# Kernel optimization log

Hardware: AMD Instinct MI355X
Metric: run time of the kernel (lower is better)

Reference implementation:

```python
import jax, jax.numpy as jnp
import numpy as np

DIM = 1024
HEADS = 16


def setup_inputs() -> dict:
    key = jax.random.key(0)
    ks = jax.random.split(key, 5)
    x = jax.random.normal(ks[0], (2, 2048, DIM), dtype=jnp.float32)
    # nn.Linear init-like scaling
    qkv_w = jax.random.normal(ks[1], (3 * DIM, DIM), dtype=jnp.float32) * (1.0 / np.sqrt(DIM))
    qkv_b = jax.random.normal(ks[2], (3 * DIM,), dtype=jnp.float32) * 0.02
    proj_w = jax.random.normal(ks[3], (DIM, DIM), dtype=jnp.float32) * (1.0 / np.sqrt(DIM))
    proj_b = jax.random.normal(ks[4], (DIM,), dtype=jnp.float32) * 0.02
    return {"x": x, "qkv_w": qkv_w, "qkv_b": qkv_b, "proj_w": proj_w, "proj_b": proj_b}


def reference(x, qkv_w, qkv_b, proj_w, proj_b):
    B, N, C = x.shape
    H = HEADS
    Dh = C // H
    scale = Dh ** -0.5
    # qkv: [B, N, 3C] -> [3, B, H, N, Dh]
    qkv = (x @ qkv_w.T + qkv_b).reshape(B, N, 3, H, Dh).transpose(2, 0, 3, 1, 4)
    q, k, v = qkv[0], qkv[1], qkv[2]
    attn = jnp.einsum('bhnd,bhmd->bhnm', q, k) * scale
    attn = jax.nn.softmax(attn, axis=-1)
    out = jnp.einsum('bhnm,bhmd->bhnd', attn, v)  # [B, H, N, Dh]
    out = out.transpose(0, 2, 1, 3).reshape(B, N, C)
    return out @ proj_w.T + proj_b
```

## Files before the change

### kernel.cpp

```cpp
#include <hip/hip_runtime.h>
#include <stdint.h>

#define DIM    1024
#define NHEADS 16
#define DH     64
#define SEQ    2048
#define BATCH  2
#define BHEADS (BATCH * NHEADS)
#define MROWS  (BATCH * SEQ)
#define SL2E   0.18033688011112042f

typedef __attribute__((ext_vector_type(8))) short bf16x8;
typedef __attribute__((ext_vector_type(4))) float f32x4;
typedef __attribute__((ext_vector_type(16))) float f32x16;
typedef unsigned short ushort_t;

#define GLDS(gp, lp) __builtin_amdgcn_global_load_lds( \
    (__attribute__((address_space(1))) void*)(gp), \
    (__attribute__((address_space(3))) void*)(lp), 16, 0, 0)

__device__ inline ushort_t f2bf(float f) {
    unsigned u = __builtin_bit_cast(unsigned, f);
    u += 0x7FFFu + ((u >> 16) & 1u);
    return (ushort_t)(u >> 16);
}

__global__ __launch_bounds__(256) void cvt_kernel(
    const float* __restrict__ s0, const float* __restrict__ s1, const float* __restrict__ s2,
    ushort_t* __restrict__ d0, ushort_t* __restrict__ d1, ushort_t* __restrict__ d2)
{
    const int N0 = MROWS * DIM;
    const int N1 = 3 * DIM * DIM;
    const int N2 = DIM * DIM;
    int e = (blockIdx.x * 256 + threadIdx.x) << 2;
    const float* src; ushort_t* dst;
    if (e < N0)                { src = s0 + e;             dst = d0 + e; }
    else if (e < N0 + N1)      { src = s1 + (e - N0);      dst = d1 + (e - N0); }
    else if (e < N0 + N1 + N2) { src = s2 + (e - N0 - N1); dst = d2 + (e - N0 - N1); }
    else return;
    float4 f = *(const float4*)src;
    ushort4 o;
    o.x = f2bf(f.x); o.y = f2bf(f.y); o.z = f2bf(f.z); o.w = f2bf(f.w);
    *(ushort4*)dst = o;
}

__global__ __launch_bounds__(256) void qkv_gemm(
    const ushort_t* __restrict__ A, const ushort_t* __restrict__ W,
    const float* __restrict__ bias,
    ushort_t* __restrict__ Qw, ushort_t* __restrict__ Kw, ushort_t* __restrict__ Vt)
{
    __shared__ union {
        ushort_t stage[2][2][128 * 64];
        ushort_t T[128 * 136];
    } sm;

    const int tid  = threadIdx.x;
    const int lane = tid & 63;
    const int wave = tid >> 6;
    const int quad = lane >> 4;
    const int l16  = lane & 15;
    const int wm   = (wave >> 1) * 64;
    const int wn   = (wave & 1) * 64;
    const int bm   = blockIdx.x * 128;
    const int bn   = blockIdx.y * 128;
    const int Rl   = lane >> 3;
    const int pp   = lane & 7;

    f32x4 acc[4][4];
    for (int i = 0; i < 4; i++)
        for (int j = 0; j < 4; j++)
            for (int r = 0; r < 4; r++) acc[i][j][r] = 0.f;

    for (int j = 0; j < 4; j++) {
        int Rb = j * 32 + wave * 8;
        int R  = Rb + Rl;
        int c  = pp ^ (R & 7);
        GLDS(A + (size_t)(bm + R) * DIM + c * 8, sm.stage[0][0] + Rb * 64 + lane * 8);
        GLDS(W + (size_t)(bn + R) * DIM + c * 8, sm.stage[0][1] + Rb * 64 + lane * 8);
    }

    const int NT = DIM / 64;
    for (int t = 0; t < NT; t++) {
        if (t < NT - 1) {
            int kk = (t + 1) * 64;
            ushort_t* As1 = sm.stage[(t + 1) & 1][0];
            ushort_t* Bs1 = sm.stage[(t + 1) & 1][1];
            for (int j = 0; j < 4; j++) {
                int Rb = j * 32 + wave * 8;
                int R  = Rb + Rl;
                int c  = pp ^ (R & 7);
                GLDS(A + (size_t)(bm + R) * DIM + kk + c * 8, As1 + Rb * 64 + lane * 8);
                GLDS(W + (size_t)(bn + R) * DIM + kk + c * 8, Bs1 + Rb * 64 + lane * 8);
            }
            __asm volatile("s_waitcnt vmcnt(8)" ::: "memory");
        } else {
            __asm volatile("s_waitcnt vmcnt(0)" ::: "memory");
        }
        __asm volatile("s_barrier" ::: "memory");

        const ushort_t* Asb = sm.stage[t & 1][0];
        const ushort_t* Bsb = sm.stage[t & 1][1];
        for (int kh = 0; kh < 2; kh++) {
            bf16x8 a[4], b[4];
            for (int mi = 0; mi < 4; mi++) {
                int r = wm + mi * 16 + l16;
                a[mi] = *(const bf16x8*)(Asb + r * 64 + (((kh * 4 + quad) ^ (r & 7)) << 3));
            }
            for (int ni = 0; ni < 4; ni++) {
                int r = wn + ni * 16 + l16;
                b[ni] = *(const bf16x8*)(Bsb + r * 64 + (((kh * 4 + quad) ^ (r & 7)) << 3));
            }
            for (int mi = 0; mi < 4; mi++)
                for (int ni = 0; ni < 4; ni++)
                    acc[mi][ni] = __builtin_amdgcn_mfma_f32_16x16x32_bf16(a[mi], b[ni], acc[mi][ni], 0, 0, 0);
        }
        __asm volatile("s_waitcnt lgkmcnt(0)" ::: "memory");
        __asm volatile("s_barrier" ::: "memory");
    }

    const int three = bn >> 10;
    const float scale = (three == 0) ? SL2E : 1.0f;
    for (int ni = 0; ni < 4; ni++) {
        int cl   = wn + ni * 16 + l16;
        float bv = bias[bn + cl];
        for (int mi = 0; mi < 4; mi++)
            for (int reg = 0; reg < 4; reg++) {
                int r = wm + mi * 16 + quad * 4 + reg;
                sm.T[r * 136 + cl] = f2bf((acc[mi][ni][reg] + bv) * scale);
            }
    }
    __syncthreads();

    const int b = bm >> 11, npos0 = bm & 2047;
    if (three < 2) {
        int r = tid >> 1, hh = tid & 1;
        int hc = (bn + hh * 64) & 1023;
        int h  = hc >> 6;
        ushort_t* dst = (three == 0 ? Qw : Kw) + ((size_t)(b * NHEADS + h) * SEQ + npos0 + r) * DH;
        const ushort_t* srcp = sm.T + r * 136 + hh * 64;
        for (int s = 0; s < 8; s++)
            *(uint4*)(dst + s * 8) = *(const uint4*)(srcp + s * 8);
    } else {
        int c = tid & 127, hh = tid >> 7;
        int hc = (bn + c) & 1023;
        int h  = hc >> 6, d = hc & 63;
        ushort_t* dst = Vt + ((size_t)(b * NHEADS + h) * DH + d) * SEQ + npos0 + hh * 64;
        for (int s = 0; s < 8; s++) {
            union { ushort_t u[8]; uint4 v; } tmp;
            for (int k2 = 0; k2 < 8; k2++) {
                int o  = hh * 64 + s * 8 + k2;
                int po = (o & ~12) | ((o & 4) << 1) | ((o & 8) >> 1);
                tmp.u[k2] = sm.T[po * 136 + c];
            }
            *(uint4*)(dst + s * 8) = tmp.v;
        }
    }
}

struct AttnSmem {
    ushort_t Qs[128 * 64];
    ushort_t Ks[3][2][32 * 64];
    ushort_t Vs[3][64 * 64];
};
union AttnSmemU {
    AttnSmem m;
    float Lb[128][66];
};

__global__ __launch_bounds__(512, 4) void attn_kernel(
    const ushort_t* __restrict__ Qw, const ushort_t* __restrict__ Kw,
    const ushort_t* __restrict__ Vt, ushort_t* __restrict__ Ao)
{
    __shared__ AttnSmemU sh;

    const int tid  = threadIdx.x;
    const int lane = tid & 63;
    const int wave = tid >> 6;
    const int grp  = wave >> 2;
    const int wg   = wave & 3;
    const int hi   = lane >> 5;
    const int l32  = lane & 31;
    const int Rl   = lane >> 3;
    const int pp   = lane & 7;

    const int bid  = blockIdx.x + 16 * blockIdx.y;
    const int bid2 = (bid & 7) * 64 + (bid >> 3);
    const int bh   = bid2 >> 4;
    const int q0   = (bid2 & 15) * 128;

    const ushort_t* Qh = Qw + (size_t)bh * SEQ * DH;
    const ushort_t* Kh = Kw + (size_t)bh * SEQ * DH;
    const ushort_t* Vh = Vt + (size_t)bh * DH * SEQ;

    for (int j = 0; j < 2; j++) {
        int Rb = j * 64 + wave * 8;
        int R  = Rb + Rl;
        int c  = pp ^ (R & 7);
        GLDS(Qh + (size_t)(q0 + R) * DH + c * 8, sh.m.Qs + Rb * 64 + lane * 8);
    }
    {
        int R = wg * 8 + Rl;
        int c = pp ^ (R & 7);
        GLDS(Kh + (size_t)(grp * 32 + R) * DH + c * 8, sh.m.Ks[0][grp] + wg * 512 + lane * 8);
        int Rd = wave * 8 + Rl;
        int cv = pp ^ (Rd & 7);
        GLDS(Vh + (size_t)Rd * SEQ + cv * 8, sh.m.Vs[0] + wave * 512 + lane * 8);
    }

    f32x16 oacc[2], liD, SZERO;
#pragma unroll
    for (int i = 0; i < 16; i++) { oacc[0][i] = 0.f; oacc[1][i] = 0.f; liD[i] = 0.f; SZERO[i] = 0.f; }
    bf16x8 qf[4];
    bf16x8 vones;
#pragma unroll
    for (int i = 0; i < 8; i++) vones[i] = (short)0x3F80;

    const int NIT = 32;
    int cur = 0;
    for (int it = 0; it < NIT; it++) {
        if (it < NIT - 1) {
            int nb = cur + 1; if (nb == 3) nb = 0;
            int kb = (it + 1) * 64;
            int R  = wg * 8 + Rl;
            int c  = pp ^ (R & 7);
            GLDS(Kh + (size_t)(kb + grp * 32 + R) * DH + c * 8, sh.m.Ks[nb][grp] + wg * 512 + lane * 8);
            int Rd = wave * 8 + Rl;
            int cv = pp ^ (Rd & 7);
            GLDS(Vh + (size_t)Rd * SEQ + kb + cv * 8, sh.m.Vs[nb] + wg * 512 + (grp * 2048) + lane * 8);
            __asm volatile("s_waitcnt vmcnt(2)" ::: "memory");
        } else {
            __asm volatile("s_waitcnt vmcnt(0)" ::: "memory");
        }
        __asm volatile("s_barrier" ::: "memory");

        if (it == 0) {
            int qr = wg * 32 + l32;
#pragma unroll
            for (int kt = 0; kt < 4; kt++)
                qf[kt] = *(const bf16x8*)(sh.m.Qs + qr * 64 + (((2 * kt + hi) ^ (qr & 7)) << 3));
        }

        const ushort_t* Ksb = sh.m.Ks[cur][grp];
        const ushort_t* Vsb = sh.m.Vs[cur];

        f32x16 S;
        __builtin_amdgcn_s_setprio(1);
#pragma unroll
        for (int kt = 0; kt < 4; kt++) {
            bf16x8 kf = *(const bf16x8*)(Ksb + l32 * 64 + (((2 * kt + hi) ^ (l32 & 7)) << 3));
            S = __builtin_amdgcn_mfma_f32_32x32x16_bf16(kf, qf[kt], kt == 0 ? SZERO : S, 0, 0, 0);
        }
        __builtin_amdgcn_s_setprio(0);

        unsigned Dw[8];
#pragma unroll
        for (int m = 0; m < 8; m++) {
            float p0 = __builtin_amdgcn_exp2f(S[2 * m]);
            float p1 = __builtin_amdgcn_exp2f(S[2 * m + 1]);
            unsigned d;
            asm("v_cvt_pk_bf16_f32 %0, %1, %2" : "=v"(d) : "v"(p0), "v"(p1));
            Dw[m] = d;
        }
        union { unsigned u[4]; bf16x8 v; } pc0, pc1;
        pc0.u[0] = Dw[0]; pc0.u[1] = Dw[1]; pc0.u[2] = Dw[2]; pc0.u[3] = Dw[3];
        pc1.u[0] = Dw[4]; pc1.u[1] = Dw[5]; pc1.u[2] = Dw[6]; pc1.u[3] = Dw[7];
        bf16x8 pa[2] = { pc0.v, pc1.v };

        __builtin_amdgcn_s_setprio(1);
        liD = __builtin_amdgcn_mfma_f32_32x32x16_bf16(pa[0], vones, liD, 0, 0, 0);
        liD = __builtin_amdgcn_mfma_f32_32x32x16_bf16(pa[1], vones, liD, 0, 0, 0);
#pragma unroll
        for (int kt = 0; kt < 2; kt++)
#pragma unroll
            for (int dh = 0; dh < 2; dh++) {
                int dr = dh * 32 + l32;
                bf16x8 vf = *(const bf16x8*)(Vsb + dr * 64 + (((grp * 4 + 2 * kt + hi) ^ (dr & 7)) << 3));
                oacc[dh] = __builtin_amdgcn_mfma_f32_32x32x16_bf16(pa[kt], vf, oacc[dh], 0, 0, 0);
            }
        __builtin_amdgcn_s_setprio(0);

        cur++; if (cur == 3) cur = 0;
    }

    __syncthreads();

    const int b = bh >> 4, h = bh & 15;
    if (grp == 1) {
#pragma unroll
        for (int dh = 0; dh < 2; dh++)
#pragma unroll
            for (int reg = 0; reg < 16; reg++) {
                int row = wg * 32 + (reg & 3) + 8 * (reg >> 2) + 4 * hi;
                sh.Lb[row][dh * 32 + l32] = oacc[dh][reg];
            }
        if (l32 == 0) {
#pragma unroll
            for (int reg = 0; reg < 16; reg++) {
                int row = wg * 32 + (reg & 3) + 8 * (reg >> 2) + 4 * hi;
                sh.Lb[row][64] = liD[reg];
            }
        }
    }
    __syncthreads();
    if (grp == 0) {
#pragma unroll
        for (int reg = 0; reg < 16; reg++) {
            int row = wg * 32 + (reg & 3) + 8 * (reg >> 2) + 4 * hi;
            float inv = 1.0f / (liD[reg] + sh.Lb[row][64]);
            int grow = q0 + row;
#pragma unroll
            for (int dh = 0; dh < 2; dh++) {
                float o = oacc[dh][reg] + sh.Lb[row][dh * 32 + l32];
                Ao[((size_t)b * SEQ + grow) * DIM + h * 64 + dh * 32 + l32] = f2bf(o * inv);
            }
        }
    }
}

__global__ __launch_bounds__(256, 4) void proj_gemm(
    const ushort_t* __restrict__ A, const ushort_t* __restrict__ W,
    const float* __restrict__ bias, float* __restrict__ Cout)
{
    __shared__ ushort_t Asd[2][128 * 64];
    __shared__ ushort_t Bsd[2][64 * 64];

    const int tid  = threadIdx.x;
    const int lane = tid & 63;
    const int wave = tid >> 6;
    const int quad = lane >> 4;
    const int l16  = lane & 15;
    const int wm   = (wave >> 1) * 64;
    const int wn   = (wave & 1) * 32;
    const int bm   = blockIdx.x * 128;
    const int bn   = blockIdx.y * 64;
    const int Rl   = lane >> 3;
    const int pp   = lane & 7;

    f32x4 acc[4][2];
    for (int i = 0; i < 4; i++)
        for (int j = 0; j < 2; j++)
            for (int r = 0; r < 4; r++) acc[i][j][r] = 0.f;

    for (int j = 0; j < 4; j++) {
        int Rb = j * 32 + wave * 8;
        int R  = Rb + Rl;
        int c  = pp ^ (R & 7);
        GLDS(A + (size_t)(bm + R) * DIM + c * 8, Asd[0] + Rb * 64 + lane * 8);
    }
    for (int j = 0; j < 2; j++) {
        int Rb = j * 32 + wave * 8;
        int R  = Rb + Rl;
        int c  = pp ^ (R & 7);
        GLDS(W + (size_t)(bn + R) * DIM + c * 8, Bsd[0] + Rb * 64 + lane * 8);
    }

    const int NT = DIM / 64;
    for (int t = 0; t < NT; t++) {
        if (t < NT - 1) {
            int kk = (t + 1) * 64;
            ushort_t* As1 = Asd[(t + 1) & 1];
            ushort_t* Bs1 = Bsd[(t + 1) & 1];
            for (int j = 0; j < 4; j++) {
                int Rb = j * 32 + wave * 8;
                int R  = Rb + Rl;
                int c  = pp ^ (R & 7);
                GLDS(A + (size_t)(bm + R) * DIM + kk + c * 8, As1 + Rb * 64 + lane * 8);
            }
            for (int j = 0; j < 2; j++) {
                int Rb = j * 32 + wave * 8;
                int R  = Rb + Rl;
                int c  = pp ^ (R & 7);
                GLDS(W + (size_t)(bn + R) * DIM + kk + c * 8, Bs1 + Rb * 64 + lane * 8);
            }
            __asm volatile("s_waitcnt vmcnt(6)" ::: "memory");
        } else {
            __asm volatile("s_waitcnt vmcnt(0)" ::: "memory");
        }
        __asm volatile("s_barrier" ::: "memory");

        const ushort_t* Asb = Asd[t & 1];
        const ushort_t* Bsb = Bsd[t & 1];
        for (int kh = 0; kh < 2; kh++) {
            bf16x8 a[4], b[2];
            for (int mi = 0; mi < 4; mi++) {
                int r = wm + mi * 16 + l16;
                a[mi] = *(const bf16x8*)(Asb + r * 64 + (((kh * 4 + quad) ^ (r & 7)) << 3));
            }
            for (int ni = 0; ni < 2; ni++) {
                int r = wn + ni * 16 + l16;
                b[ni] = *(const bf16x8*)(Bsb + r * 64 + (((kh * 4 + quad) ^ (r & 7)) << 3));
            }
            for (int mi = 0; mi < 4; mi++)
                for (int ni = 0; ni < 2; ni++)
                    acc[mi][ni] = __builtin_amdgcn_mfma_f32_16x16x32_bf16(a[mi], b[ni], acc[mi][ni], 0, 0, 0);
        }
        __asm volatile("s_waitcnt lgkmcnt(0)" ::: "memory");
        __asm volatile("s_barrier" ::: "memory");
    }

    for (int mi = 0; mi < 4; mi++) {
        for (int ni = 0; ni < 2; ni++) {
            int col  = bn + wn + ni * 16 + l16;
            float bv = bias[col];
            for (int reg = 0; reg < 4; reg++) {
                int row = bm + wm + mi * 16 + quad * 4 + reg;
                Cout[(size_t)row * DIM + col] = acc[mi][ni][reg] + bv;
            }
        }
    }
}

extern "C" void kernel_launch(void* const* d_in, const int* in_sizes, int n_in,
                              void* d_out, int out_size, void* d_ws, size_t ws_size,
                              hipStream_t stream) {
    const float* x      = (const float*)d_in[0];
    const float* qkv_w  = (const float*)d_in[1];
    const float* qkv_b  = (const float*)d_in[2];
    const float* proj_w = (const float*)d_in[3];
    const float* proj_b = (const float*)d_in[4];
    float* out = (float*)d_out;

    ushort_t* xb      = (ushort_t*)d_ws;
    ushort_t* qkv_wb  = xb      + (size_t)MROWS * DIM;
    ushort_t* proj_wb = qkv_wb  + (size_t)3 * DIM * DIM;
    ushort_t* Qw      = proj_wb + (size_t)DIM * DIM;
    ushort_t* Kw      = Qw      + (size_t)BHEADS * SEQ * DH;
    ushort_t* Vt      = Kw      + (size_t)BHEADS * SEQ * DH;
    ushort_t* Ao      = Vt      + (size_t)BHEADS * SEQ * DH;

    const int total_cvt = MROWS * DIM + 3 * DIM * DIM + DIM * DIM;
    cvt_kernel<<<total_cvt / (4 * 256), 256, 0, stream>>>(x, qkv_w, proj_w, xb, qkv_wb, proj_wb);
    qkv_gemm<<<dim3(MROWS / 128, (3 * DIM) / 128), 256, 0, stream>>>(xb, qkv_wb, qkv_b, Qw, Kw, Vt);
    attn_kernel<<<dim3(SEQ / 128, BHEADS), 512, 0, stream>>>(Qw, Kw, Vt, Ao);
    proj_gemm<<<dim3(MROWS / 128, DIM / 64), 256, 0, stream>>>(Ao, proj_wb, proj_b, out);
}
```

Measured before the change: 177.2 us.

## Double-buffer 128-key tiles in attention loop instead of triple-buffered 64-key tiles

The attention kernel's K/V staging moves from a three-stage ring of 64-key tiles to a two-stage double buffer of 128-key tiles. The loop runs 16 iterations instead of 32, each processing two 32-key sub-blocks per wave group. This halves the number of barriers and loop-control overheads. The load for the next tile is now issued after a full vmcnt(0) wait and barrier, which gives less prefetch depth. LDS use grows from about 56KB to 80KB, which may reduce occupancy against the launch bound of 4 blocks.

```diff
diff --git a/kernel.cpp b/kernel.cpp
--- a/kernel.cpp
+++ b/kernel.cpp
@@ -159,8 +159,8 @@
 
 struct AttnSmem {
     ushort_t Qs[128 * 64];
-    ushort_t Ks[3][2][32 * 64];
-    ushort_t Vs[3][64 * 64];
+    ushort_t Ks[2][2][64 * 64];
+    ushort_t Vs[2][64 * 128];
 };
 union AttnSmemU {
     AttnSmem m;
@@ -199,12 +199,18 @@
         GLDS(Qh + (size_t)(q0 + R) * DH + c * 8, sh.m.Qs + Rb * 64 + lane * 8);
     }
     {
-        int R = wg * 8 + Rl;
-        int c = pp ^ (R & 7);
-        GLDS(Kh + (size_t)(grp * 32 + R) * DH + c * 8, sh.m.Ks[0][grp] + wg * 512 + lane * 8);
-        int Rd = wave * 8 + Rl;
-        int cv = pp ^ (Rd & 7);
-        GLDS(Vh + (size_t)Rd * SEQ + cv * 8, sh.m.Vs[0] + wave * 512 + lane * 8);
+        for (int j = 0; j < 2; j++) {
+            int R = wg * 16 + j * 8 + Rl;
+            int c = pp ^ (R & 7);
+            GLDS(Kh + (size_t)(grp * 64 + R) * DH + c * 8,
+                 sh.m.Ks[0][grp] + (wg * 16 + j * 8) * 64 + lane * 8);
+        }
+        for (int j = 0; j < 2; j++) {
+            int Rv = wave * 8 + j * 4 + (lane >> 4);
+            int ck = lane & 15;
+            GLDS(Vh + (size_t)Rv * SEQ + (ck ^ (Rv & 7)) * 8,
+                 sh.m.Vs[0] + (wave * 8 + j * 4) * 128 + lane * 8);
+        }
     }
 
     f32x16 oacc[2], liD, SZERO;
@@ -215,23 +221,27 @@
 #pragma unroll
     for (int i = 0; i < 8; i++) vones[i] = (short)0x3F80;
 
-    const int NIT = 32;
-    int cur = 0;
+    const int NIT = 16;
     for (int it = 0; it < NIT; it++) {
+        __asm volatile("s_waitcnt vmcnt(0)" ::: "memory");
+        __asm volatile("s_barrier" ::: "memory");
+
         if (it < NIT - 1) {
-            int nb = cur + 1; if (nb == 3) nb = 0;
-            int kb = (it + 1) * 64;
-            int R  = wg * 8 + Rl;
-            int c  = pp ^ (R & 7);
-            GLDS(Kh + (size_t)(kb + grp * 32 + R) * DH + c * 8, sh.m.Ks[nb][grp] + wg * 512 + lane * 8);
-            int Rd = wave * 8 + Rl;
-            int cv = pp ^ (Rd & 7);
-            GLDS(Vh + (size_t)Rd * SEQ + kb + cv * 8, sh.m.Vs[nb] + wg * 512 + (grp * 2048) + lane * 8);
-            __asm volatile("s_waitcnt vmcnt(2)" ::: "memory");
-        } else {
-            __asm volatile("s_waitcnt vmcnt(0)" ::: "memory");
-        }
-        __asm volatile("s_barrier" ::: "memory");
+            int nb = (it + 1) & 1;
+            int kb = (it + 1) * 128;
+            for (int j = 0; j < 2; j++) {
+                int R = wg * 16 + j * 8 + Rl;
+                int c = pp ^ (R & 7);
+                GLDS(Kh + (size_t)(kb + grp * 64 + R) * DH + c * 8,
+                     sh.m.Ks[nb][grp] + (wg * 16 + j * 8) * 64 + lane * 8);
+            }
+            for (int j = 0; j < 2; j++) {
+                int Rv = wave * 8 + j * 4 + (lane >> 4);
+                int ck = lane & 15;
+                GLDS(Vh + (size_t)Rv * SEQ + kb + (ck ^ (Rv & 7)) * 8,
+                     sh.m.Vs[nb] + (wave * 8 + j * 4) * 128 + lane * 8);
+            }
+        }
 
         if (it == 0) {
             int qr = wg * 32 + l32;
@@ -240,46 +250,48 @@
                 qf[kt] = *(const bf16x8*)(sh.m.Qs + qr * 64 + (((2 * kt + hi) ^ (qr & 7)) << 3));
         }
 
-        const ushort_t* Ksb = sh.m.Ks[cur][grp];
-        const ushort_t* Vsb = sh.m.Vs[cur];
-
-        f32x16 S;
-        __builtin_amdgcn_s_setprio(1);
-#pragma unroll
-        for (int kt = 0; kt < 4; kt++) {
-            bf16x8 kf = *(const bf16x8*)(Ksb + l32 * 64 + (((2 * kt + hi) ^ (l32 & 7)) << 3));
-            S = __builtin_amdgcn_mfma_f32_32x32x16_bf16(kf, qf[kt], kt == 0 ? SZERO : S, 0, 0, 0);
-        }
-        __builtin_amdgcn_s_setprio(0);
-
-        unsigned Dw[8];
-#pragma unroll
-        for (int m = 0; m < 8; m++) {
-            float p0 = __builtin_amdgcn_exp2f(S[2 * m]);
-            float p1 = __builtin_amdgcn_exp2f(S[2 * m + 1]);
-            unsigned d;
-            asm("v_cvt_pk_bf16_f32 %0, %1, %2" : "=v"(d) : "v"(p0), "v"(p1));
-            Dw[m] = d;
-        }
-        union { unsigned u[4]; bf16x8 v; } pc0, pc1;
-        pc0.u[0] = Dw[0]; pc0.u[1] = Dw[1]; pc0.u[2] = Dw[2]; pc0.u[3] = Dw[3];
-        pc1.u[0] = Dw[4]; pc1.u[1] = Dw[5]; pc1.u[2] = Dw[6]; pc1.u[3] = Dw[7];
-        bf16x8 pa[2] = { pc0.v, pc1.v };
-
-        __builtin_amdgcn_s_setprio(1);
-        liD = __builtin_amdgcn_mfma_f32_32x32x16_bf16(pa[0], vones, liD, 0, 0, 0);
-        liD = __builtin_amdgcn_mfma_f32_32x32x16_bf16(pa[1], vones, liD, 0, 0, 0);
-#pragma unroll
-        for (int kt = 0; kt < 2; kt++)
-#pragma unroll
-            for (int dh = 0; dh < 2; dh++) {
-                int dr = dh * 32 + l32;
-                bf16x8 vf = *(const bf16x8*)(Vsb + dr * 64 + (((grp * 4 + 2 * kt + hi) ^ (dr & 7)) << 3));
-                oacc[dh] = __builtin_amdgcn_mfma_f32_32x32x16_bf16(pa[kt], vf, oacc[dh], 0, 0, 0);
-            }
-        __builtin_amdgcn_s_setprio(0);
-
-        cur++; if (cur == 3) cur = 0;
+        const ushort_t* Ksb = sh.m.Ks[it & 1][grp];
+        const ushort_t* Vsb = sh.m.Vs[it & 1];
+
+#pragma unroll
+        for (int ks = 0; ks < 2; ks++) {
+            f32x16 S;
+            __builtin_amdgcn_s_setprio(1);
+#pragma unroll
+            for (int kt = 0; kt < 4; kt++) {
+                bf16x8 kf = *(const bf16x8*)(Ksb + (ks * 32 + l32) * 64 + (((2 * kt + hi) ^ (l32 & 7)) << 3));
+                S = __builtin_amdgcn_mfma_f32_32x32x16_bf16(kf, qf[kt], kt == 0 ? SZERO : S, 0, 0, 0);
+            }
+            __builtin_amdgcn_s_setprio(0);
+
+            unsigned Dw[8];
+#pragma unroll
+            for (int m = 0; m < 8; m++) {
+                float p0 = __builtin_amdgcn_exp2f(S[2 * m]);
+                float p1 = __builtin_amdgcn_exp2f(S[2 * m + 1]);
+                unsigned d;
+                asm("v_cvt_pk_bf16_f32 %0, %1, %2" : "=v"(d) : "v"(p0), "v"(p1));
+                Dw[m] = d;
+            }
+            union { unsigned u[4]; bf16x8 v; } pc0, pc1;
+            pc0.u[0] = Dw[0]; pc0.u[1] = Dw[1]; pc0.u[2] = Dw[2]; pc0.u[3] = Dw[3];
+            pc1.u[0] = Dw[4]; pc1.u[1] = Dw[5]; pc1.u[2] = Dw[6]; pc1.u[3] = Dw[7];
+            bf16x8 pa[2] = { pc0.v, pc1.v };
+
+            __builtin_amdgcn_s_setprio(1);
+            liD = __builtin_amdgcn_mfma_f32_32x32x16_bf16(pa[0], vones, liD, 0, 0, 0);
+            liD = __builtin_amdgcn_mfma_f32_32x32x16_bf16(pa[1], vones, liD, 0, 0, 0);
+#pragma unroll
+            for (int kt = 0; kt < 2; kt++)
+#pragma unroll
+                for (int dh = 0; dh < 2; dh++) {
+                    int dr = dh * 32 + l32;
+                    int jc = grp * 8 + ks * 4 + 2 * kt + hi;
+                    bf16x8 vf = *(const bf16x8*)(Vsb + dr * 128 + ((jc ^ (l32 & 7)) << 3));
+                    oacc[dh] = __builtin_amdgcn_mfma_f32_32x32x16_bf16(pa[kt], vf, oacc[dh], 0, 0, 0);
+                }
+            __builtin_amdgcn_s_setprio(0);
+        }
     }
 
     __syncthreads();
```

Measured after the change: 178.4 us. Within noise of the previous version (+0.6%).

## Alias Q staging into the third K/V buffer to shrink attention LDS

Applied to the files above, without the earlier changes.

Flattens attention shared memory into one buffer where the Q tile shares space with the third K/V ring slot. Q fragments are loaded into registers before the loop, and tiles 0 and 1 are prefetched up front so slot 2 is free to overwrite. This cuts LDS per block from 64KB to 48KB, and the launch bound is raised to allow higher occupancy. The tighter register budget may cause spills, and with only 512 blocks the extra resident blocks per CU may add little.

```diff
diff --git a/kernel.cpp b/kernel.cpp
--- a/kernel.cpp
+++ b/kernel.cpp
@@ -157,21 +157,14 @@
     }
 }
 
-struct AttnSmem {
-    ushort_t Qs[128 * 64];
-    ushort_t Ks[3][2][32 * 64];
-    ushort_t Vs[3][64 * 64];
-};
-union AttnSmemU {
-    AttnSmem m;
-    float Lb[128][66];
-};
-
-__global__ __launch_bounds__(512, 4) void attn_kernel(
+__global__ __launch_bounds__(512, 6) void attn_kernel(
     const ushort_t* __restrict__ Qw, const ushort_t* __restrict__ Kw,
     const ushort_t* __restrict__ Vt, ushort_t* __restrict__ Ao)
 {
-    __shared__ AttnSmemU sh;
+    __shared__ union {
+        ushort_t u[24576];
+        float Lb[128][66];
+    } sh;
 
     const int tid  = threadIdx.x;
     const int lane = tid & 63;
@@ -192,25 +185,39 @@
     const ushort_t* Kh = Kw + (size_t)bh * SEQ * DH;
     const ushort_t* Vh = Vt + (size_t)bh * DH * SEQ;
 
+    ushort_t* const Qs = sh.u + 16384;
+
     for (int j = 0; j < 2; j++) {
         int Rb = j * 64 + wave * 8;
         int R  = Rb + Rl;
         int c  = pp ^ (R & 7);
-        GLDS(Qh + (size_t)(q0 + R) * DH + c * 8, sh.m.Qs + Rb * 64 + lane * 8);
-    }
-    {
+        GLDS(Qh + (size_t)(q0 + R) * DH + c * 8, Qs + Rb * 64 + lane * 8);
+    }
+    for (int t = 0; t < 2; t++) {
         int R = wg * 8 + Rl;
         int c = pp ^ (R & 7);
-        GLDS(Kh + (size_t)(grp * 32 + R) * DH + c * 8, sh.m.Ks[0][grp] + wg * 512 + lane * 8);
+        GLDS(Kh + (size_t)(t * 64 + grp * 32 + R) * DH + c * 8,
+             sh.u + (t << 13) + grp * 2048 + wg * 512 + lane * 8);
         int Rd = wave * 8 + Rl;
         int cv = pp ^ (Rd & 7);
-        GLDS(Vh + (size_t)Rd * SEQ + cv * 8, sh.m.Vs[0] + wave * 512 + lane * 8);
-    }
+        GLDS(Vh + (size_t)Rd * SEQ + t * 64 + cv * 8,
+             sh.u + (t << 13) + 4096 + wave * 512 + lane * 8);
+    }
+    __asm volatile("s_waitcnt vmcnt(2)" ::: "memory");
+    __asm volatile("s_barrier" ::: "memory");
+
+    bf16x8 qf[4];
+    {
+        int qr = wg * 32 + l32;
+#pragma unroll
+        for (int kt = 0; kt < 4; kt++)
+            qf[kt] = *(const bf16x8*)(Qs + qr * 64 + (((2 * kt + hi) ^ (qr & 7)) << 3));
+    }
+    __asm volatile("s_waitcnt lgkmcnt(0)" ::: "memory");
 
     f32x16 oacc[2], liD, SZERO;
 #pragma unroll
     for (int i = 0; i < 16; i++) { oacc[0][i] = 0.f; oacc[1][i] = 0.f; liD[i] = 0.f; SZERO[i] = 0.f; }
-    bf16x8 qf[4];
     bf16x8 vones;
 #pragma unroll
     for (int i = 0; i < 8; i++) vones[i] = (short)0x3F80;
@@ -218,30 +225,27 @@
     const int NIT = 32;
     int cur = 0;
     for (int it = 0; it < NIT; it++) {
-        if (it < NIT - 1) {
+        if (it >= 1 && it < NIT - 1) {
             int nb = cur + 1; if (nb == 3) nb = 0;
             int kb = (it + 1) * 64;
             int R  = wg * 8 + Rl;
             int c  = pp ^ (R & 7);
-            GLDS(Kh + (size_t)(kb + grp * 32 + R) * DH + c * 8, sh.m.Ks[nb][grp] + wg * 512 + lane * 8);
+            GLDS(Kh + (size_t)(kb + grp * 32 + R) * DH + c * 8,
+                 sh.u + (nb << 13) + grp * 2048 + wg * 512 + lane * 8);
             int Rd = wave * 8 + Rl;
             int cv = pp ^ (Rd & 7);
-            GLDS(Vh + (size_t)Rd * SEQ + kb + cv * 8, sh.m.Vs[nb] + wg * 512 + (grp * 2048) + lane * 8);
+            GLDS(Vh + (size_t)Rd * SEQ + kb + cv * 8,
+                 sh.u + (nb << 13) + 4096 + wave * 512 + lane * 8);
+        }
+        if (it < NIT - 1) {
             __asm volatile("s_waitcnt vmcnt(2)" ::: "memory");
         } else {
             __asm volatile("s_waitcnt vmcnt(0)" ::: "memory");
         }
         __asm volatile("s_barrier" ::: "memory");
 
-        if (it == 0) {
-            int qr = wg * 32 + l32;
-#pragma unroll
-            for (int kt = 0; kt < 4; kt++)
-                qf[kt] = *(const bf16x8*)(sh.m.Qs + qr * 64 + (((2 * kt + hi) ^ (qr & 7)) << 3));
-        }
-
-        const ushort_t* Ksb = sh.m.Ks[cur][grp];
-        const ushort_t* Vsb = sh.m.Vs[cur];
+        const ushort_t* Ksb = sh.u + (cur << 13) + grp * 2048;
+        const ushort_t* Vsb = sh.u + (cur << 13) + 4096;
 
         f32x16 S;
         __builtin_amdgcn_s_setprio(1);
```

Result: slower. 260.4 us (+46.9%).
